# Kernel tuning notes

Measured on AMD Instinct MI355X. Metric: run time of the kernel, lower is better.

The kernel has to match this reference:

```python
import jax, jax.numpy as jnp
import numpy as np

N_NODES = 50000
N_EDGES = 800000
D_IN = 128
D_HID = 128
N_LAYERS = 3
BN_EPS = 1e-5


def setup_inputs() -> dict:
    key = jax.random.key(0)
    ks = jax.random.split(key, 12)
    x = jax.random.normal(ks[0], (N_NODES, D_IN), dtype=jnp.float32)
    edge_index = jax.random.randint(ks[1], (2, N_EDGES), 0, N_NODES, dtype=jnp.int64)
    edge_weight = jax.random.uniform(ks[2], (N_EDGES,), dtype=jnp.float32)
    s1 = 1.0 / np.sqrt(D_IN)
    s2 = 1.0 / np.sqrt(D_HID)
    # stacked per-layer GIN MLP params (layer 0 in_dim == hidden_dim so stacking is valid)
    W1s = jax.random.uniform(ks[3], (N_LAYERS, D_HID, D_HID), jnp.float32, -s1, s1)
    b1s = jax.random.uniform(ks[4], (N_LAYERS, D_HID), jnp.float32, -s1, s1)
    W2s = jax.random.uniform(ks[5], (N_LAYERS, D_HID, D_HID), jnp.float32, -s2, s2)
    b2s = jax.random.uniform(ks[6], (N_LAYERS, D_HID), jnp.float32, -s2, s2)
    eps = jnp.zeros((N_LAYERS,), jnp.float32)  # GINConv eps init 0
    gamma = jnp.ones((D_HID,), jnp.float32)
    beta = jnp.zeros((D_HID,), jnp.float32)
    Wp = jax.random.uniform(ks[7], (D_HID, D_HID), jnp.float32, -s2, s2)
    bp = jax.random.uniform(ks[8], (D_HID,), jnp.float32, -s2, s2)
    prelu_a = jnp.asarray(0.25, jnp.float32)
    return {"x": x, "edge_weight": edge_weight, "W1s": W1s, "b1s": b1s,
            "W2s": W2s, "b2s": b2s, "eps": eps, "gamma": gamma, "beta": beta,
            "Wp": Wp, "bp": bp, "prelu_a": prelu_a, "edge_index": edge_index}


def reference(x, edge_weight, W1s, b1s, W2s, b2s, eps, gamma, beta, Wp, bp, prelu_a, edge_index):
    src, dst = edge_index[0], edge_index[1]
    z = x
    for i in range(N_LAYERS):
        # GINConv: sum-aggregate weighted neighbor messages, then 2-layer MLP
        msg = z[src] * edge_weight[:, None]                       # [E, d]
        agg = jax.ops.segment_sum(msg, dst, num_segments=N_NODES)  # [N, d]
        h = (1.0 + eps[i]) * z + agg
        h = jax.nn.relu(h @ W1s[i] + b1s[i]) @ W2s[i] + b2s[i]
        z = jax.nn.relu(h)  # activation; dropout inactive (eval)
    # BatchNorm1d (training-mode batch statistics, biased variance)
    mean = jnp.mean(z, axis=0)
    var = jnp.var(z, axis=0)
    zn = (z - mean) * jax.lax.rsqrt(var + BN_EPS) * gamma + beta
    # projection head: Linear -> PReLU (dropout inactive)
    p = zn @ Wp + bp
    p = jnp.where(p >= 0, p, prelu_a * p)
    return zn, p
```

## Files before the change

### kernel.cpp

```cpp
#include <hip/hip_runtime.h>
#include <hip/hip_fp16.h>

#define N_NODES 50000
#define N_EDGES 800000
#define D 128
#define ND (N_NODES * D)
#define BN_EPS 1e-5f

#define NB 256
#define NPB 196
#define BCAP 4096

typedef short bf16x8 __attribute__((ext_vector_type(8)));
typedef _Float16 f16x8 __attribute__((ext_vector_type(8)));
typedef float f32x4 __attribute__((ext_vector_type(4)));
typedef unsigned short u16x8 __attribute__((ext_vector_type(8)));

__device__ inline unsigned short f2bf(float f) {
    unsigned int u = __float_as_uint(f);
    u += 0x7FFF + ((u >> 16) & 1);
    return (unsigned short)(u >> 16);
}
__device__ inline float bf2f(unsigned short h) {
    return __uint_as_float(((unsigned int)h) << 16);
}
__device__ inline unsigned short f2h(float f) {
    return __half_as_ushort(__float2half(f));
}
__device__ inline float h2f(unsigned short u) {
    return __half2float(__ushort_as_half(u));
}
__device__ inline f16x8 as_f16x8(u16x8 v) {
    union { u16x8 u; f16x8 f; } x; x.u = v; return x.f;
}
__device__ inline bf16x8 as_bf16x8(u16x8 v) {
    union { u16x8 u; bf16x8 f; } x; x.u = v; return x.f;
}

__global__ void convert_x(const float* __restrict__ x, ushort* __restrict__ xh) {
    int i = (blockIdx.x * blockDim.x + threadIdx.x) * 4;
    if (i < ND) {
        float4 v = *(const float4*)(x + i);
        *(ushort4*)(xh + i) = make_ushort4(f2h(v.x), f2h(v.y), f2h(v.z), f2h(v.w));
    }
}

__global__ void pack_w_split(const float* __restrict__ W1s, const float* __restrict__ W2s,
                             const float* __restrict__ Wp, ushort* __restrict__ out) {
    int idx = blockIdx.x * blockDim.x + threadIdx.x;
    if (idx >= 7 * 16384) return;
    int m = idx >> 14;
    int p = idx & 16383;
    int c = p >> 11;
    int kc = (p >> 9) & 3;
    int lane = (p >> 3) & 63;
    int j = p & 7;
    int k = kc * 32 + (lane >> 4) * 8 + j;
    int col = c * 16 + (lane & 15);
    const float* src = (m < 3) ? (W1s + (size_t)m * 16384)
                     : (m < 6) ? (W2s + (size_t)(m - 3) * 16384)
                               : Wp;
    float v = src[k * 128 + col];
    if (m < 3) {
        unsigned short hi = f2h(v);
        float r = (v - h2f(hi)) * 2048.0f;
        out[(size_t)(2 * m) * 16384 + p] = hi;
        out[(size_t)(2 * m + 1) * 16384 + p] = f2h(r);
    } else {
        unsigned short hi = f2bf(v);
        float r = v - bf2f(hi);
        out[(size_t)(2 * m) * 16384 + p] = hi;
        out[(size_t)(2 * m + 1) * 16384 + p] = f2bf(r);
    }
}

__global__ __launch_bounds__(256) void bhist_kernel(const int* __restrict__ dst,
                                                    int* __restrict__ gbcnt) {
    __shared__ int cnt[NB];
    int tid = threadIdx.x;
    cnt[tid] = 0;
    __syncthreads();
    int base = blockIdx.x * 2048;
    #pragma unroll
    for (int k = 0; k < 8; ++k) {
        int e = base + k * 256 + tid;
        if (e < N_EDGES) atomicAdd(&cnt[dst[e] / NPB], 1);
    }
    __syncthreads();
    int c = cnt[tid];
    if (c > 0) atomicAdd(&gbcnt[tid], c);
}

__global__ __launch_bounds__(256) void bscan_kernel(const int* __restrict__ gbcnt,
                                                    int* __restrict__ bstart,
                                                    int* __restrict__ bcur) {
    __shared__ int s[NB];
    int tid = threadIdx.x;
    int v = gbcnt[tid];
    s[tid] = v;
    __syncthreads();
    for (int d = 1; d < NB; d <<= 1) {
        int t = (tid >= d) ? s[tid - d] : 0;
        __syncthreads();
        s[tid] += t;
        __syncthreads();
    }
    int incl = s[tid];
    bstart[tid] = incl - v;
    bcur[tid] = incl - v;
    if (tid == NB - 1) bstart[NB] = incl;
}

__global__ __launch_bounds__(256) void bucket_scatter(
    const int* __restrict__ src, const int* __restrict__ dst,
    const float* __restrict__ ew, int* __restrict__ bcur,
    uint2* __restrict__ pay) {
    __shared__ int cnt[NB];
    __shared__ int cur[NB];
    int tid = threadIdx.x;
    for (int i = tid; i < NB; i += 256) cnt[i] = 0;
    __syncthreads();
    int base = blockIdx.x * 2048;
    int s[8], d[8], b[8];
    float w[8];
    #pragma unroll
    for (int k = 0; k < 8; ++k) {
        int e = base + k * 256 + tid;
        bool v = e < N_EDGES;
        d[k] = v ? dst[e] : 0;
        s[k] = v ? src[e] : 0;
        w[k] = v ? ew[e] : 0.f;
        b[k] = d[k] / NPB;
        if (v) atomicAdd(&cnt[b[k]], 1);
    }
    __syncthreads();
    for (int i = tid; i < NB; i += 256) {
        int c = cnt[i];
        cur[i] = (c > 0) ? atomicAdd(&bcur[i], c) : 0;
    }
    __syncthreads();
    #pragma unroll
    for (int k = 0; k < 8; ++k) {
        int e = base + k * 256 + tid;
        if (e < N_EDGES) {
            int bk = b[k];
            int p = atomicAdd(&cur[bk], 1);
            unsigned dloc = (unsigned)(d[k] - bk * NPB);
            pay[p] = make_uint2((unsigned)s[k] | (dloc << 17), __float_as_uint(w[k]));
        }
    }
}

__global__ __launch_bounds__(256) void bucket_sort(const int* __restrict__ bstart,
                                                   int* __restrict__ offs,
                                                   uint2* __restrict__ pay) {
    __shared__ uint2 lp[BCAP];
    __shared__ int lcnt[NB];
    __shared__ int cur[NPB];
    int b = blockIdx.x;
    int tid = threadIdx.x;
    int n0 = b * NPB;
    int n1 = min(n0 + NPB, N_NODES);
    int nn = n1 - n0;
    int r0 = bstart[b];
    int r1 = bstart[b + 1];
    int cnt = r1 - r0;
    lcnt[tid] = 0;
    __syncthreads();
    for (int i = tid; i < cnt; i += 256) {
        uint2 e = pay[r0 + i];
        if (i < BCAP) lp[i] = e;
        atomicAdd(&lcnt[e.x >> 17], 1);
    }
    __syncthreads();
    int v = lcnt[tid];
    for (int d = 1; d < NB; d <<= 1) {
        int t = (tid >= d) ? lcnt[tid - d] : 0;
        __syncthreads();
        lcnt[tid] += t;
        __syncthreads();
    }
    int excl = lcnt[tid] - v;
    if (tid < nn) {
        offs[n0 + tid] = r0 + excl;
        cur[tid] = excl;
    }
    if (tid == 0) offs[n1] = r1;
    __syncthreads();
    for (int i = tid; i < cnt; i += 256) {
        if (i < BCAP) {
            uint2 e = lp[i];
            int p = atomicAdd(&cur[e.x >> 17], 1);
            if (p < BCAP) pay[r0 + p] = make_uint2(e.x & 0x1FFFFu, e.y);
        }
    }
}

__global__ void gather_agg_f16(const ushort* __restrict__ z, const int* __restrict__ offs,
                               const uint2* __restrict__ pay,
                               const float* __restrict__ epsp, int layer,
                               ushort* __restrict__ A) {
    int tid = blockIdx.x * blockDim.x + threadIdx.x;
    int n = tid >> 5;
    if (n >= N_NODES) return;
    int f = (tid & 31) << 2;
    float epsv = 1.0f + epsp[layer];
    int beg = offs[n], end = offs[n + 1];
    ushort4 zi = *(const ushort4*)(z + (size_t)n * D + f);
    float ax = epsv * h2f(zi.x), ay = epsv * h2f(zi.y);
    float az = epsv * h2f(zi.z), aw = epsv * h2f(zi.w);
    int j = beg;
    for (; j + 4 <= end; j += 4) {
        uint2 e0 = pay[j];
        uint2 e1 = pay[j + 1];
        uint2 e2 = pay[j + 2];
        uint2 e3 = pay[j + 3];
        ushort4 v0 = *(const ushort4*)(z + (size_t)e0.x * D + f);
        ushort4 v1 = *(const ushort4*)(z + (size_t)e1.x * D + f);
        ushort4 v2 = *(const ushort4*)(z + (size_t)e2.x * D + f);
        ushort4 v3 = *(const ushort4*)(z + (size_t)e3.x * D + f);
        float w0 = __uint_as_float(e0.y);
        float w1 = __uint_as_float(e1.y);
        float w2 = __uint_as_float(e2.y);
        float w3 = __uint_as_float(e3.y);
        ax += h2f(v0.x) * w0 + h2f(v1.x) * w1 + h2f(v2.x) * w2 + h2f(v3.x) * w3;
        ay += h2f(v0.y) * w0 + h2f(v1.y) * w1 + h2f(v2.y) * w2 + h2f(v3.y) * w3;
        az += h2f(v0.z) * w0 + h2f(v1.z) * w1 + h2f(v2.z) * w2 + h2f(v3.z) * w3;
        aw += h2f(v0.w) * w0 + h2f(v1.w) * w1 + h2f(v2.w) * w2 + h2f(v3.w) * w3;
    }
    for (; j < end; ++j) {
        uint2 e0 = pay[j];
        ushort4 v0 = *(const ushort4*)(z + (size_t)e0.x * D + f);
        float w0 = __uint_as_float(e0.y);
        ax += h2f(v0.x) * w0; ay += h2f(v0.y) * w0;
        az += h2f(v0.z) * w0; aw += h2f(v0.w) * w0;
    }
    *(ushort4*)(A + (size_t)n * D + f) = make_ushort4(f2h(ax), f2h(ay), f2h(az), f2h(aw));
}

#define HSTR2 136
template<bool STATS>
__global__ __launch_bounds__(256) void mlp_fused(
    const ushort* __restrict__ A,
    const ushort* __restrict__ W1hi, const ushort* __restrict__ W1lo,
    const float* __restrict__ b1,
    const ushort* __restrict__ W2hi, const ushort* __restrict__ W2lo,
    const float* __restrict__ b2, ushort* __restrict__ Z,
    float* __restrict__ stats) {
    __shared__ ushort Hhi[64 * HSTR2];
    __shared__ ushort Hlo[64 * HSTR2];
    int tid = threadIdx.x;
    int lane = tid & 63;
    int wave = tid >> 6;
    int rlo = lane & 15;
    int quad = lane >> 4;
    int blk0 = blockIdx.x * 64;

    const f16x8* W1h = (const f16x8*)W1hi;
    const f16x8* W1l = (const f16x8*)W1lo;
    const bf16x8* W2h = (const bf16x8*)W2hi;
    const bf16x8* W2l = (const bf16x8*)W2lo;

    f16x8 af[4][4];
    #pragma unroll
    for (int rf = 0; rf < 4; ++rf) {
        int arow = blk0 + rf * 16 + rlo;
        int ar = (arow < N_NODES) ? arow : (N_NODES - 1);
        #pragma unroll
        for (int kc = 0; kc < 4; ++kc) {
            u16x8 raw = *(const u16x8*)(A + (size_t)ar * D + kc * 32 + quad * 8);
            af[rf][kc] = as_f16x8(raw);
        }
    }

    #pragma unroll
    for (int cc = 0; cc < 2; ++cc) {
        int c = 2 * wave + cc;
        f32x4 aH[4], aL[4];
        #pragma unroll
        for (int rf = 0; rf < 4; ++rf) {
            aH[rf] = (f32x4){0.f, 0.f, 0.f, 0.f};
            aL[rf] = (f32x4){0.f, 0.f, 0.f, 0.f};
        }
        #pragma unroll
        for (int kc = 0; kc < 4; ++kc) {
            f16x8 wh = W1h[(c * 4 + kc) * 64 + lane];
            f16x8 wl = W1l[(c * 4 + kc) * 64 + lane];
            #pragma unroll
            for (int rf = 0; rf < 4; ++rf) {
                aH[rf] = __builtin_amdgcn_mfma_f32_16x16x32_f16(af[rf][kc], wh, aH[rf], 0, 0, 0);
                aL[rf] = __builtin_amdgcn_mfma_f32_16x16x32_f16(af[rf][kc], wl, aL[rf], 0, 0, 0);
            }
        }
        int col = c * 16 + rlo;
        float bb = b1[col];
        #pragma unroll
        for (int rf = 0; rf < 4; ++rf) {
            #pragma unroll
            for (int r = 0; r < 4; ++r) {
                float v = fmaxf(aH[rf][r] + aL[rf][r] * (1.0f / 2048.0f) + bb, 0.f);
                unsigned short h = f2bf(v);
                int idx = (rf * 16 + quad * 4 + r) * HSTR2 + col;
                Hhi[idx] = h;
                Hlo[idx] = f2bf(v - bf2f(h));
            }
        }
    }
    __syncthreads();

    f32x4 acc2[2][4];
    #pragma unroll
    for (int cc = 0; cc < 2; ++cc)
        #pragma unroll
        for (int rf = 0; rf < 4; ++rf)
            acc2[cc][rf] = (f32x4){0.f, 0.f, 0.f, 0.f};

    #pragma unroll
    for (int kc = 0; kc < 4; ++kc) {
        bf16x8 a2hi[4], a2lo[4];
        #pragma unroll
        for (int rf = 0; rf < 4; ++rf) {
            int idx = (rf * 16 + rlo) * HSTR2 + kc * 32 + quad * 8;
            a2hi[rf] = as_bf16x8(*(const u16x8*)&Hhi[idx]);
            a2lo[rf] = as_bf16x8(*(const u16x8*)&Hlo[idx]);
        }
        #pragma unroll
        for (int cc = 0; cc < 2; ++cc) {
            int c = 2 * wave + cc;
            bf16x8 wh = W2h[(c * 4 + kc) * 64 + lane];
            bf16x8 wl = W2l[(c * 4 + kc) * 64 + lane];
            #pragma unroll
            for (int rf = 0; rf < 4; ++rf) {
                acc2[cc][rf] = __builtin_amdgcn_mfma_f32_16x16x32_bf16(a2lo[rf], wh, acc2[cc][rf], 0, 0, 0);
                acc2[cc][rf] = __builtin_amdgcn_mfma_f32_16x16x32_bf16(a2hi[rf], wl, acc2[cc][rf], 0, 0, 0);
                acc2[cc][rf] = __builtin_amdgcn_mfma_f32_16x16x32_bf16(a2hi[rf], wh, acc2[cc][rf], 0, 0, 0);
            }
        }
    }
    __syncthreads();

    #pragma unroll
    for (int cc = 0; cc < 2; ++cc) {
        int c = 2 * wave + cc;
        int col = c * 16 + rlo;
        float bb = b2[col];
        float s = 0.f, s2 = 0.f;
        #pragma unroll
        for (int rf = 0; rf < 4; ++rf) {
            #pragma unroll
            for (int r = 0; r < 4; ++r) {
                float v = fmaxf(acc2[cc][rf][r] + bb, 0.f);
                Hhi[(rf * 16 + quad * 4 + r) * HSTR2 + col] = f2h(v);
                if (STATS) {
                    float m = (blk0 + rf * 16 + quad * 4 + r < N_NODES) ? v : 0.f;
                    s += m;
                    s2 += m * m;
                }
            }
        }
        if (STATS) {
            s  += __shfl_xor(s, 16, 64);
            s  += __shfl_xor(s, 32, 64);
            s2 += __shfl_xor(s2, 16, 64);
            s2 += __shfl_xor(s2, 32, 64);
            if (quad == 0) {
                atomicAdd(&stats[col], s);
                atomicAdd(&stats[D + col], s2);
            }
        }
    }
    __syncthreads();

    #pragma unroll
    for (int it = 0; it < 4; ++it) {
        int r = wave * 16 + it * 4 + quad;
        int grow = blk0 + r;
        if (grow < N_NODES) {
            u16x8 vv = *(const u16x8*)&Hhi[r * HSTR2 + rlo * 8];
            *(u16x8*)(Z + (size_t)grow * D + rlo * 8) = vv;
        }
    }
}

#define PSTR 132
__global__ __launch_bounds__(256) void bn_proj(
    const ushort* __restrict__ Z, const float* __restrict__ stats,
    const float* __restrict__ gamma, const float* __restrict__ beta,
    const ushort* __restrict__ Wphi, const ushort* __restrict__ Wplo,
    const float* __restrict__ bp, const float* __restrict__ prelu_a,
    float* __restrict__ zn_out, float* __restrict__ p_out) {
    __shared__ float sc_s[D];
    __shared__ float sh_s[D];
    __shared__ float Ps[4][16 * PSTR];
    int tid = threadIdx.x;
    int lane = tid & 63;
    int wave = tid >> 6;
    int rlo = lane & 15;
    int quad = lane >> 4;

    if (tid < D) {
        float m = stats[tid] * (1.0f / N_NODES);
        float v = stats[D + tid] * (1.0f / N_NODES) - m * m;
        float rs = rsqrtf(v + BN_EPS);
        float sc = rs * gamma[tid];
        sc_s[tid] = sc;
        sh_s[tid] = beta[tid] - m * sc;
    }
    __syncthreads();

    int row0 = blockIdx.x * 64 + wave * 16;
    int arow = row0 + rlo;
    int ar = (arow < N_NODES) ? arow : (N_NODES - 1);

    const bf16x8* Wh = (const bf16x8*)Wphi;
    const bf16x8* Wl = (const bf16x8*)Wplo;

    bf16x8 ahi[4], alo[4];
    #pragma unroll
    for (int kc = 0; kc < 4; ++kc) {
        u16x8 raw = *(const u16x8*)(Z + (size_t)ar * D + kc * 32 + quad * 8);
        float zn[8];
        #pragma unroll
        for (int j = 0; j < 8; ++j) {
            int k = kc * 32 + quad * 8 + j;
            zn[j] = sc_s[k] * h2f(raw[j]) + sh_s[k];
            unsigned short h = f2bf(zn[j]);
            ahi[kc][j] = (short)h;
            alo[kc][j] = (short)f2bf(zn[j] - bf2f(h));
        }
        if (arow < N_NODES) {
            float* dst = zn_out + (size_t)arow * D + kc * 32 + quad * 8;
            *(float4*)dst = make_float4(zn[0], zn[1], zn[2], zn[3]);
            *(float4*)(dst + 4) = make_float4(zn[4], zn[5], zn[6], zn[7]);
        }
    }

    f32x4 acc[8];
    #pragma unroll
    for (int c = 0; c < 8; ++c) acc[c] = (f32x4){0.f, 0.f, 0.f, 0.f};
    #pragma unroll
    for (int c = 0; c < 8; ++c) {
        #pragma unroll
        for (int kc = 0; kc < 4; ++kc) {
            bf16x8 wh = Wh[(c * 4 + kc) * 64 + lane];
            bf16x8 wl = Wl[(c * 4 + kc) * 64 + lane];
            acc[c] = __builtin_amdgcn_mfma_f32_16x16x32_bf16(alo[kc], wh, acc[c], 0, 0, 0);
            acc[c] = __builtin_amdgcn_mfma_f32_16x16x32_bf16(ahi[kc], wl, acc[c], 0, 0, 0);
            acc[c] = __builtin_amdgcn_mfma_f32_16x16x32_bf16(ahi[kc], wh, acc[c], 0, 0, 0);
        }
    }

    float aP = prelu_a[0];
    #pragma unroll
    for (int c = 0; c < 8; ++c) {
        int col = c * 16 + rlo;
        float bb = bp[col];
        #pragma unroll
        for (int r = 0; r < 4; ++r) {
            float v = acc[c][r] + bb;
            v = (v >= 0.f) ? v : aP * v;
            Ps[wave][(quad * 4 + r) * PSTR + col] = v;
        }
    }
    __syncthreads();
    #pragma unroll
    for (int p2 = 0; p2 < 8; ++p2) {
        int r = p2 * 2 + (lane >> 5);
        int grow = row0 + r;
        if (grow < N_NODES) {
            *(float4*)(p_out + (size_t)grow * D + (lane & 31) * 4) =
                *(const float4*)&Ps[wave][r * PSTR + (lane & 31) * 4];
        }
    }
}

extern "C" void kernel_launch(void* const* d_in, const int* in_sizes, int n_in,
                              void* d_out, int out_size, void* d_ws, size_t ws_size,
                              hipStream_t stream) {
    (void)in_sizes; (void)n_in; (void)out_size; (void)ws_size;
    const float* x     = (const float*)d_in[0];
    const float* ew    = (const float*)d_in[1];
    const float* W1s   = (const float*)d_in[2];
    const float* b1s   = (const float*)d_in[3];
    const float* W2s   = (const float*)d_in[4];
    const float* b2s   = (const float*)d_in[5];
    const float* eps   = (const float*)d_in[6];
    const float* gamma = (const float*)d_in[7];
    const float* beta  = (const float*)d_in[8];
    const float* Wp    = (const float*)d_in[9];
    const float* bp    = (const float*)d_in[10];
    const float* pa    = (const float*)d_in[11];
    const int*   ei    = (const int*)d_in[12];
    const int* srcp = ei;
    const int* dstp = ei + N_EDGES;

    char* wsb = (char*)d_ws;
    float*  stats  = (float*)wsb;                 wsb += 1024;
    int*    offs   = (int*)wsb;                   wsb += 200016;
    int*    bcur   = (int*)wsb;
    int*    gbcnt  = bcur + 256;
    int*    bstart = bcur + 512;                  wsb += 200016;
    uint2*  pay    = (uint2*)wsb;                 wsb += 6400000;
    ushort* Wpk    = (ushort*)wsb;                wsb += 14 * 16384 * 2;
    ushort* Xh     = (ushort*)wsb;                wsb += (size_t)ND * 2;
    ushort* Ah     = (ushort*)wsb;                wsb += (size_t)ND * 2;
    ushort* Zh     = (ushort*)wsb;                wsb += (size_t)ND * 2;

    float* out_zn = (float*)d_out;
    float* out_p  = out_zn + ND;

    hipMemsetAsync(stats, 0, 256 * sizeof(float), stream);
    hipMemsetAsync(gbcnt, 0, NB * sizeof(int), stream);

    convert_x<<<(ND / 4 + 255) / 256, 256, 0, stream>>>(x, Xh);
    pack_w_split<<<(7 * 16384 + 255) / 256, 256, 0, stream>>>(W1s, W2s, Wp, Wpk);

    bhist_kernel<<<(N_EDGES + 2047) / 2048, 256, 0, stream>>>(dstp, gbcnt);
    bscan_kernel<<<1, 256, 0, stream>>>(gbcnt, bstart, bcur);
    bucket_scatter<<<(N_EDGES + 2047) / 2048, 256, 0, stream>>>(srcp, dstp, ew, bcur, pay);
    bucket_sort<<<NB, 256, 0, stream>>>(bstart, offs, pay);

    int mgrid = (N_NODES + 63) / 64;
    const ushort* zin = Xh;
    for (int l = 0; l < 3; ++l) {
        gather_agg_f16<<<(N_NODES * 32 + 255) / 256, 256, 0, stream>>>(zin, offs, pay, eps, l, Ah);
        if (l < 2) {
            mlp_fused<false><<<mgrid, 256, 0, stream>>>(Ah,
                Wpk + (size_t)(2 * l) * 16384,       Wpk + (size_t)(2 * l + 1) * 16384, b1s + (size_t)l * D,
                Wpk + (size_t)(2 * (3 + l)) * 16384, Wpk + (size_t)(2 * (3 + l) + 1) * 16384, b2s + (size_t)l * D,
                Zh, stats);
        } else {
            mlp_fused<true><<<mgrid, 256, 0, stream>>>(Ah,
                Wpk + (size_t)(2 * l) * 16384,       Wpk + (size_t)(2 * l + 1) * 16384, b1s + (size_t)l * D,
                Wpk + (size_t)(2 * (3 + l)) * 16384, Wpk + (size_t)(2 * (3 + l) + 1) * 16384, b2s + (size_t)l * D,
                Zh, stats);
        }
        zin = Zh;
    }
    bn_proj<<<mgrid, 256, 0, stream>>>(Zh, stats, gamma, beta,
        Wpk + (size_t)12 * 16384, Wpk + (size_t)13 * 16384, bp, pa, out_zn, out_p);
}
```

Baseline: 371.1 us.

## Fuse neighbor aggregation into GIN MLP kernel via shared-memory tile

The separate gather/aggregate kernel is folded into the MLP kernel: each 256-thread block now aggregates its 64 nodes into a shared-memory tile and feeds the MFMA stage from it. This removes the global round trip of the aggregated activations and one launch per layer. Because a layer now reads and writes node features in the same kernel, the features ping-pong between two buffers. The cost is less gather parallelism per block, with 8 rounds of 8 nodes serialized, more shared memory per block, and possibly lower occupancy for the latency-bound gather.

Result: slower. 452.2 us (+21.8%).

```diff
diff --git a/kernel.cpp b/kernel.cpp
--- a/kernel.cpp
+++ b/kernel.cpp
@@ -196,57 +196,17 @@
     }
 }
 
-__global__ void gather_agg_f16(const ushort* __restrict__ z, const int* __restrict__ offs,
-                               const uint2* __restrict__ pay,
-                               const float* __restrict__ epsp, int layer,
-                               ushort* __restrict__ A) {
-    int tid = blockIdx.x * blockDim.x + threadIdx.x;
-    int n = tid >> 5;
-    if (n >= N_NODES) return;
-    int f = (tid & 31) << 2;
-    float epsv = 1.0f + epsp[layer];
-    int beg = offs[n], end = offs[n + 1];
-    ushort4 zi = *(const ushort4*)(z + (size_t)n * D + f);
-    float ax = epsv * h2f(zi.x), ay = epsv * h2f(zi.y);
-    float az = epsv * h2f(zi.z), aw = epsv * h2f(zi.w);
-    int j = beg;
-    for (; j + 4 <= end; j += 4) {
-        uint2 e0 = pay[j];
-        uint2 e1 = pay[j + 1];
-        uint2 e2 = pay[j + 2];
-        uint2 e3 = pay[j + 3];
-        ushort4 v0 = *(const ushort4*)(z + (size_t)e0.x * D + f);
-        ushort4 v1 = *(const ushort4*)(z + (size_t)e1.x * D + f);
-        ushort4 v2 = *(const ushort4*)(z + (size_t)e2.x * D + f);
-        ushort4 v3 = *(const ushort4*)(z + (size_t)e3.x * D + f);
-        float w0 = __uint_as_float(e0.y);
-        float w1 = __uint_as_float(e1.y);
-        float w2 = __uint_as_float(e2.y);
-        float w3 = __uint_as_float(e3.y);
-        ax += h2f(v0.x) * w0 + h2f(v1.x) * w1 + h2f(v2.x) * w2 + h2f(v3.x) * w3;
-        ay += h2f(v0.y) * w0 + h2f(v1.y) * w1 + h2f(v2.y) * w2 + h2f(v3.y) * w3;
-        az += h2f(v0.z) * w0 + h2f(v1.z) * w1 + h2f(v2.z) * w2 + h2f(v3.z) * w3;
-        aw += h2f(v0.w) * w0 + h2f(v1.w) * w1 + h2f(v2.w) * w2 + h2f(v3.w) * w3;
-    }
-    for (; j < end; ++j) {
-        uint2 e0 = pay[j];
-        ushort4 v0 = *(const ushort4*)(z + (size_t)e0.x * D + f);
-        float w0 = __uint_as_float(e0.y);
-        ax += h2f(v0.x) * w0; ay += h2f(v0.y) * w0;
-        az += h2f(v0.z) * w0; aw += h2f(v0.w) * w0;
-    }
-    *(ushort4*)(A + (size_t)n * D + f) = make_ushort4(f2h(ax), f2h(ay), f2h(az), f2h(aw));
-}
-
 #define HSTR2 136
 template<bool STATS>
-__global__ __launch_bounds__(256) void mlp_fused(
-    const ushort* __restrict__ A,
+__global__ __launch_bounds__(256) void gin_fused(
+    const ushort* __restrict__ z, const int* __restrict__ offs,
+    const uint2* __restrict__ pay, const float* __restrict__ epsp, int layer,
     const ushort* __restrict__ W1hi, const ushort* __restrict__ W1lo,
     const float* __restrict__ b1,
     const ushort* __restrict__ W2hi, const ushort* __restrict__ W2lo,
     const float* __restrict__ b2, ushort* __restrict__ Z,
     float* __restrict__ stats) {
+    __shared__ ushort Af[64 * HSTR2];
     __shared__ ushort Hhi[64 * HSTR2];
     __shared__ ushort Hlo[64 * HSTR2];
     int tid = threadIdx.x;
@@ -256,6 +216,51 @@
     int quad = lane >> 4;
     int blk0 = blockIdx.x * 64;
 
+    {
+        int group = tid >> 5;
+        int f = (tid & 31) << 2;
+        float epsv = 1.0f + epsp[layer];
+        #pragma unroll 2
+        for (int round = 0; round < 8; ++round) {
+            int nl = round * 8 + group;
+            int n = blk0 + nl;
+            int nc = (n < N_NODES) ? n : (N_NODES - 1);
+            int beg = offs[nc], end = offs[nc + 1];
+            ushort4 zi = *(const ushort4*)(z + (size_t)nc * D + f);
+            float ax = epsv * h2f(zi.x), ay = epsv * h2f(zi.y);
+            float az = epsv * h2f(zi.z), aw = epsv * h2f(zi.w);
+            int j = beg;
+            for (; j + 4 <= end; j += 4) {
+                uint2 e0 = pay[j];
+                uint2 e1 = pay[j + 1];
+                uint2 e2 = pay[j + 2];
+                uint2 e3 = pay[j + 3];
+                ushort4 v0 = *(const ushort4*)(z + (size_t)e0.x * D + f);
+                ushort4 v1 = *(const ushort4*)(z + (size_t)e1.x * D + f);
+                ushort4 v2 = *(const ushort4*)(z + (size_t)e2.x * D + f);
+                ushort4 v3 = *(const ushort4*)(z + (size_t)e3.x * D + f);
+                float w0 = __uint_as_float(e0.y);
+                float w1 = __uint_as_float(e1.y);
+                float w2 = __uint_as_float(e2.y);
+                float w3 = __uint_as_float(e3.y);
+                ax += h2f(v0.x) * w0 + h2f(v1.x) * w1 + h2f(v2.x) * w2 + h2f(v3.x) * w3;
+                ay += h2f(v0.y) * w0 + h2f(v1.y) * w1 + h2f(v2.y) * w2 + h2f(v3.y) * w3;
+                az += h2f(v0.z) * w0 + h2f(v1.z) * w1 + h2f(v2.z) * w2 + h2f(v3.z) * w3;
+                aw += h2f(v0.w) * w0 + h2f(v1.w) * w1 + h2f(v2.w) * w2 + h2f(v3.w) * w3;
+            }
+            for (; j < end; ++j) {
+                uint2 e0 = pay[j];
+                ushort4 v0 = *(const ushort4*)(z + (size_t)e0.x * D + f);
+                float w0 = __uint_as_float(e0.y);
+                ax += h2f(v0.x) * w0; ay += h2f(v0.y) * w0;
+                az += h2f(v0.z) * w0; aw += h2f(v0.w) * w0;
+            }
+            *(ushort4*)&Af[nl * HSTR2 + f] =
+                make_ushort4(f2h(ax), f2h(ay), f2h(az), f2h(aw));
+        }
+    }
+    __syncthreads();
+
     const f16x8* W1h = (const f16x8*)W1hi;
     const f16x8* W1l = (const f16x8*)W1lo;
     const bf16x8* W2h = (const bf16x8*)W2hi;
@@ -264,12 +269,9 @@
     f16x8 af[4][4];
     #pragma unroll
     for (int rf = 0; rf < 4; ++rf) {
-        int arow = blk0 + rf * 16 + rlo;
-        int ar = (arow < N_NODES) ? arow : (N_NODES - 1);
         #pragma unroll
         for (int kc = 0; kc < 4; ++kc) {
-            u16x8 raw = *(const u16x8*)(A + (size_t)ar * D + kc * 32 + quad * 8);
-            af[rf][kc] = as_f16x8(raw);
+            af[rf][kc] = as_f16x8(*(const u16x8*)&Af[(rf * 16 + rlo) * HSTR2 + kc * 32 + quad * 8]);
         }
     }
 
@@ -503,8 +505,8 @@
     uint2*  pay    = (uint2*)wsb;                 wsb += 6400000;
     ushort* Wpk    = (ushort*)wsb;                wsb += 14 * 16384 * 2;
     ushort* Xh     = (ushort*)wsb;                wsb += (size_t)ND * 2;
-    ushort* Ah     = (ushort*)wsb;                wsb += (size_t)ND * 2;
-    ushort* Zh     = (ushort*)wsb;                wsb += (size_t)ND * 2;
+    ushort* Za     = (ushort*)wsb;                wsb += (size_t)ND * 2;
+    ushort* Zb     = (ushort*)wsb;                wsb += (size_t)ND * 2;
 
     float* out_zn = (float*)d_out;
     float* out_p  = out_zn + ND;
@@ -522,21 +524,22 @@
 
     int mgrid = (N_NODES + 63) / 64;
     const ushort* zin = Xh;
+    ushort* zout = Za;
     for (int l = 0; l < 3; ++l) {
-        gather_agg_f16<<<(N_NODES * 32 + 255) / 256, 256, 0, stream>>>(zin, offs, pay, eps, l, Ah);
         if (l < 2) {
-            mlp_fused<false><<<mgrid, 256, 0, stream>>>(Ah,
+            gin_fused<false><<<mgrid, 256, 0, stream>>>(zin, offs, pay, eps, l,
                 Wpk + (size_t)(2 * l) * 16384,       Wpk + (size_t)(2 * l + 1) * 16384, b1s + (size_t)l * D,
                 Wpk + (size_t)(2 * (3 + l)) * 16384, Wpk + (size_t)(2 * (3 + l) + 1) * 16384, b2s + (size_t)l * D,
-                Zh, stats);
+                zout, stats);
         } else {
-            mlp_fused<true><<<mgrid, 256, 0, stream>>>(Ah,
+            gin_fused<true><<<mgrid, 256, 0, stream>>>(zin, offs, pay, eps, l,
                 Wpk + (size_t)(2 * l) * 16384,       Wpk + (size_t)(2 * l + 1) * 16384, b1s + (size_t)l * D,
                 Wpk + (size_t)(2 * (3 + l)) * 16384, Wpk + (size_t)(2 * (3 + l) + 1) * 16384, b2s + (size_t)l * D,
-                Zh, stats);
-        }
-        zin = Zh;
-    }
-    bn_proj<<<mgrid, 256, 0, stream>>>(Zh, stats, gamma, beta,
+                zout, stats);
+        }
+        zin = zout;
+        zout = (zout == Za) ? Zb : Za;
+    }
+    bn_proj<<<mgrid, 256, 0, stream>>>(zin, stats, gamma, beta,
         Wpk + (size_t)12 * 16384, Wpk + (size_t)13 * 16384, bp, pa, out_zn, out_p);
 }
```
